# Performance work log

Hardware: AMD Instinct MI355X
Metric: run time of the kernel (lower is better)

Reference implementation:

```python
import jax, jax.numpy as jnp
import numpy as np

EMBED = 1024
HEADS = 16
HEAD_DIM = EMBED // HEADS


def setup_inputs() -> dict:
    key = jax.random.key(0)
    ks = jax.random.split(key, 12)
    B, S = 2, 2048
    inp = {
        "query": jax.random.normal(ks[0], (B, S, EMBED), dtype=jnp.float32),
        "key": jax.random.normal(ks[1], (B, S, EMBED), dtype=jnp.float32),
        "value": jax.random.normal(ks[2], (B, S, EMBED), dtype=jnp.float32),
        "mask": jnp.ones((B, 1, 1, S), dtype=jnp.int32),
    }
    scale = 1.0 / np.sqrt(EMBED)
    inp["Wq"] = jax.random.normal(ks[3], (EMBED, EMBED), dtype=jnp.float32) * scale
    inp["bq"] = jax.random.normal(ks[4], (EMBED,), dtype=jnp.float32) * 0.01
    inp["Wk"] = jax.random.normal(ks[5], (EMBED, EMBED), dtype=jnp.float32) * scale
    inp["bk"] = jax.random.normal(ks[6], (EMBED,), dtype=jnp.float32) * 0.01
    inp["Wv"] = jax.random.normal(ks[7], (EMBED, EMBED), dtype=jnp.float32) * scale
    inp["bv"] = jax.random.normal(ks[8], (EMBED,), dtype=jnp.float32) * 0.01
    inp["Wo"] = jax.random.normal(ks[9], (EMBED, EMBED), dtype=jnp.float32) * scale
    inp["bo"] = jax.random.normal(ks[10], (EMBED,), dtype=jnp.float32) * 0.01
    return inp


def reference(query, key, value, mask, Wq, bq, Wk, bk, Wv, bv, Wo, bo):
    N, Lq, _ = query.shape
    Lk = key.shape[1]
    # Linear projections (torch Linear: x @ W.T + b)
    q = (query @ Wq.T + bq).reshape(N, Lq, HEADS, HEAD_DIM)
    k = (key @ Wk.T + bk).reshape(N, Lk, HEADS, HEAD_DIM)
    v = (value @ Wv.T + bv).reshape(N, Lk, HEADS, HEAD_DIM)
    # scores: [N, H, Lq, Lk]
    energy = jnp.einsum("nqhd,nkhd->nhqk", q, k)
    energy = jnp.where(mask == 0, jnp.float32(-1e20), energy)
    # NOTE: original scales by sqrt(embedSize), not sqrt(head_dim)
    attn = jax.nn.softmax(energy / jnp.sqrt(jnp.float32(EMBED)), axis=3)
    out = jnp.einsum("nhqv,nvhd->nqhd", attn, v).reshape(N, Lq, EMBED)
    return out @ Wo.T + bo
```

## Files before the change

kernel.cpp:

```cpp
#include <hip/hip_runtime.h>
#include <stdint.h>

typedef unsigned short u16;
typedef __attribute__((ext_vector_type(8))) short short8;
typedef __attribute__((ext_vector_type(4))) short short4v;
typedef __attribute__((ext_vector_type(4))) float floatx4;
typedef __attribute__((ext_vector_type(16))) float floatx16;
typedef __attribute__((ext_vector_type(2))) unsigned int uint2v;
typedef __attribute__((ext_vector_type(4))) unsigned int uint4v;

#define AS_GLOBAL __attribute__((address_space(1)))
#define AS_LDS    __attribute__((address_space(3)))

#define QSCALE 0.045084220f

__device__ __forceinline__ float bf2f(u16 u) {
  union { unsigned int i; float f; } x; x.i = ((unsigned int)u) << 16; return x.f;
}
__device__ __forceinline__ u16 f2bf(float f) {
  union { float f; unsigned int i; } x; x.f = f;
  unsigned int u = x.i;
  u += 0x7fffu + ((u >> 16) & 1u);
  return (u16)(u >> 16);
}
__device__ __forceinline__ u16 f2bf_fast(float f) {
  union { float f; unsigned int i; } x; x.f = f;
  return (u16)((x.i + 0x8000u) >> 16);
}

__device__ __forceinline__ unsigned int cvtpk_bf16(float lo, float hi) {
  unsigned int w;
  __asm__("v_cvt_pk_bf16_f32 %0, %1, %2" : "=v"(w) : "v"(lo), "v"(hi));
  return w;
}

__device__ __forceinline__ void pl32_swap(unsigned int& a, unsigned int& b) {
#if __has_builtin(__builtin_amdgcn_permlane32_swap)
  uint2v r = __builtin_amdgcn_permlane32_swap(a, b, false, false);
  a = r[0]; b = r[1];
#else
  __asm__("v_permlane32_swap_b32 %0, %1" : "+v"(a), "+v"(b));
#endif
}

__device__ __forceinline__ int probe_is_f32(const void* p) {
  const unsigned int* w = (const unsigned int*)p;
  int cnt = 0;
#pragma unroll
  for (int i = 0; i < 64; ++i) {
    unsigned int lo = w[i] & 0xFFFFu;
    int e = (int)((lo >> 7) & 0xFFu);
    cnt += (e >= 117 && e <= 137) ? 1 : 0;
  }
  return cnt < 32;
}

__device__ __forceinline__ short8 ld8(const void* P, size_t off, int isf32) {
  if (isf32) {
    const float* q = (const float*)P + off;
    float4 x = *(const float4*)q;
    float4 y = *(const float4*)(q + 4);
    short8 r;
    r[0] = (short)f2bf(x.x); r[1] = (short)f2bf(x.y);
    r[2] = (short)f2bf(x.z); r[3] = (short)f2bf(x.w);
    r[4] = (short)f2bf(y.x); r[5] = (short)f2bf(y.y);
    r[6] = (short)f2bf(y.z); r[7] = (short)f2bf(y.w);
    return r;
  }
  return *(const short8*)((const u16*)P + off);
}

__device__ __forceinline__ float ldscalar(const void* P, size_t idx, int isf32) {
  return isf32 ? ((const float*)P)[idx] : bf2f(((const u16*)P)[idx]);
}

__global__ __launch_bounds__(256) void cvt7(
    const void* s0, const void* s1, const void* s2, const void* s3,
    const void* s4, const void* s5, const void* s6,
    u16* d0, u16* d1, u16* d2, u16* d3, u16* d4, u16* d5, u16* d6)
{
  const int z = blockIdx.y;
  const void* src; u16* dst; int n;
  switch (z) {
    case 0: src = s0; dst = d0; n = 4194304; break;
    case 1: src = s1; dst = d1; n = 4194304; break;
    case 2: src = s2; dst = d2; n = 4194304; break;
    case 3: src = s3; dst = d3; n = 1048576; break;
    case 4: src = s4; dst = d4; n = 1048576; break;
    case 5: src = s5; dst = d5; n = 1048576; break;
    default: src = s6; dst = d6; n = 1048576; break;
  }
  const int isf32 = probe_is_f32(src);
  for (int i = blockIdx.x * 256 + threadIdx.x; i * 4 < n; i += gridDim.x * 256) {
    if (isf32) {
      float4 x = ((const float4*)src)[i];
      short4v r;
      r[0] = (short)f2bf(x.x); r[1] = (short)f2bf(x.y);
      r[2] = (short)f2bf(x.z); r[3] = (short)f2bf(x.w);
      *(short4v*)(dst + (size_t)i * 4) = r;
    } else {
      *(short4v*)(dst + (size_t)i * 4) = ((const short4v*)src)[i];
    }
  }
}

__device__ __forceinline__ void gemm_core_bf16(
    const u16* __restrict__ A, const u16* __restrict__ W,
    u16* As, u16* Bs, floatx4 acc[4][4], int m0, int n0, int K, int tid)
{
  const int lane = tid & 63, wv = tid >> 6;
  const int wm = wv >> 1, wn = wv & 1;
  const int g = lane >> 4, ml = lane & 15;
  const int r0 = tid >> 2, kc = (tid & 3) << 3;
  const u16* Ag0 = A + (size_t)(m0 + r0) * K + kc;
  const u16* Ag1 = A + (size_t)(m0 + r0 + 64) * K + kc;
  const u16* Bg0 = W + (size_t)(n0 + r0) * K + kc;
  const u16* Bg1 = W + (size_t)(n0 + r0 + 64) * K + kc;

#define STAGE_QKV(buf_, kt_) do {                                              \
    u16* a0 = As + (buf_) * 4096 + tid * 8;                                    \
    u16* b0 = Bs + (buf_) * 4096 + tid * 8;                                    \
    __builtin_amdgcn_global_load_lds((const AS_GLOBAL unsigned int*)(Ag0 + (kt_)), \
                                     (AS_LDS unsigned int*)a0, 16, 0, 0);      \
    __builtin_amdgcn_global_load_lds((const AS_GLOBAL unsigned int*)(Ag1 + (kt_)), \
                                     (AS_LDS unsigned int*)(a0 + 2048), 16, 0, 0); \
    __builtin_amdgcn_global_load_lds((const AS_GLOBAL unsigned int*)(Bg0 + (kt_)), \
                                     (AS_LDS unsigned int*)b0, 16, 0, 0);      \
    __builtin_amdgcn_global_load_lds((const AS_GLOBAL unsigned int*)(Bg1 + (kt_)), \
                                     (AS_LDS unsigned int*)(b0 + 2048), 16, 0, 0); \
  } while (0)

  STAGE_QKV(0, 0);
  int buf = 0;
#pragma unroll 2
  for (int kt = 0; kt < K; kt += 32) {
    const int nk = (kt + 32 < K) ? (kt + 32) : 0;
    STAGE_QKV(buf ^ 1, nk);
    __asm__ __volatile__("s_waitcnt vmcnt(4)\n\ts_barrier" ::: "memory");
    const u16* Ac = As + buf * 4096;
    const u16* Bc = Bs + buf * 4096;
    short8 af[4], bf[4];
#pragma unroll
    for (int i = 0; i < 4; ++i)
      af[i] = *(const short8*)(Ac + (wm * 64 + i * 16 + ml) * 32 + g * 8);
#pragma unroll
    for (int j = 0; j < 4; ++j)
      bf[j] = *(const short8*)(Bc + (wn * 64 + j * 16 + ml) * 32 + g * 8);
#pragma unroll
    for (int i = 0; i < 4; ++i)
#pragma unroll
      for (int j = 0; j < 4; ++j)
        acc[i][j] = __builtin_amdgcn_mfma_f32_16x16x32_bf16(af[i], bf[j], acc[i][j], 0, 0, 0);
    __asm__ __volatile__("s_waitcnt lgkmcnt(0)\n\ts_barrier" ::: "memory");
    buf ^= 1;
  }
#undef STAGE_QKV
  __asm__ __volatile__("s_waitcnt vmcnt(0)" ::: "memory");
}

__device__ __forceinline__ void gemm_core_cvt(
    const void* __restrict__ A, const void* __restrict__ W, int aF32, int bF32,
    u16* As, u16* Bs, floatx4 acc[4][4], int m0, int n0, int K, int tid)
{
  const int lane = tid & 63, wv = tid >> 6;
  const int wm = wv >> 1, wn = wv & 1;
  const int g = lane >> 4, ml = lane & 15;
  const int r0 = tid >> 2, kc = (tid & 3) << 3;
  const size_t offA0 = (size_t)(m0 + r0) * K + kc;
  const size_t offA1 = (size_t)(m0 + r0 + 64) * K + kc;
  const size_t offB0 = (size_t)(n0 + r0) * K + kc;
  const size_t offB1 = (size_t)(n0 + r0 + 64) * K + kc;
  u16* Al0 = As + tid * 8;  u16* Al1 = As + (tid + 256) * 8;
  u16* Bl0 = Bs + tid * 8;  u16* Bl1 = Bs + (tid + 256) * 8;
  for (int kt = 0; kt < K; kt += 32) {
    short8 a0 = ld8(A, offA0 + kt, aF32);
    short8 a1 = ld8(A, offA1 + kt, aF32);
    short8 b0 = ld8(W, offB0 + kt, bF32);
    short8 b1 = ld8(W, offB1 + kt, bF32);
    *(short8*)Al0 = a0;  *(short8*)Al1 = a1;
    *(short8*)Bl0 = b0;  *(short8*)Bl1 = b1;
    __syncthreads();
    short8 af[4], bf[4];
#pragma unroll
    for (int i = 0; i < 4; ++i)
      af[i] = *(const short8*)(As + (wm * 64 + i * 16 + ml) * 32 + g * 8);
#pragma unroll
    for (int j = 0; j < 4; ++j)
      bf[j] = *(const short8*)(Bs + (wn * 64 + j * 16 + ml) * 32 + g * 8);
#pragma unroll
    for (int i = 0; i < 4; ++i)
#pragma unroll
      for (int j = 0; j < 4; ++j)
        acc[i][j] = __builtin_amdgcn_mfma_f32_16x16x32_bf16(af[i], bf[j], acc[i][j], 0, 0, 0);
    __syncthreads();
  }
}

__device__ __forceinline__ void qkv_epilogue(
    floatx4 acc[4][4], const void* Bi, int cF32, u16* O, int m0, int n0,
    int tid, int z)
{
  const int lane = tid & 63, wv = tid >> 6;
  const int wm = wv >> 1, wn = wv & 1, g = lane >> 4, ml = lane & 15;
  const float sc = (z == 0) ? QSCALE : 1.0f;
#pragma unroll
  for (int j = 0; j < 4; ++j) {
    int gn = n0 + wn * 64 + j * 16 + ml;
    float bvv = ldscalar(Bi, (size_t)gn, cF32);
    int h = gn >> 6, d = gn & 63;
    if (z == 2) {
#pragma unroll
      for (int i = 0; i < 4; ++i) {
        int gm0 = m0 + wm * 64 + i * 16 + g * 4;
        int b = gm0 >> 11, s0 = gm0 & 2047;
        short4v pk;
#pragma unroll
        for (int r = 0; r < 4; ++r) pk[r] = (short)f2bf_fast(acc[i][j][r] + bvv);
        *(short4v*)(O + ((((size_t)b * 16 + h) * 64 + d) * 2048 + s0)) = pk;
      }
    } else {
#pragma unroll
      for (int i = 0; i < 4; ++i)
#pragma unroll
        for (int r = 0; r < 4; ++r) {
          int gm = m0 + wm * 64 + i * 16 + g * 4 + r;
          int b = gm >> 11, s = gm & 2047;
          O[(((size_t)b * 16 + h) * 2048 + s) * 64 + d] =
              f2bf_fast((acc[i][j][r] + bvv) * sc);
        }
    }
  }
}

__global__ __launch_bounds__(256) void qkv_gemm_bf16(
    const u16* __restrict__ Xq, const u16* __restrict__ Xk, const u16* __restrict__ Xv,
    const u16* __restrict__ Wq, const u16* __restrict__ Wk, const u16* __restrict__ Wv,
    const void* __restrict__ Bq, const void* __restrict__ Bk, const void* __restrict__ Bv,
    u16* __restrict__ Oq, u16* __restrict__ Ok, u16* __restrict__ Ov)
{
  __align__(16) __shared__ u16 As[8192];
  __align__(16) __shared__ u16 Bs[8192];
  const int z = blockIdx.z;
  const u16* X = (z == 0) ? Xq : (z == 1) ? Xk : Xv;
  const u16* W = (z == 0) ? Wq : (z == 1) ? Wk : Wv;
  const void* Bi = (z == 0) ? Bq : (z == 1) ? Bk : Bv;
  u16* O = (z == 0) ? Oq : (z == 1) ? Ok : Ov;
  const int tid = threadIdx.x;
  const int m0 = blockIdx.x * 128, n0 = blockIdx.y * 128;
  floatx4 acc[4][4] = {};
  gemm_core_bf16(X, W, As, Bs, acc, m0, n0, 1024, tid);
  const int cF32 = probe_is_f32(Bi);
  qkv_epilogue(acc, Bi, cF32, O, m0, n0, tid, z);
}

__global__ __launch_bounds__(256) void qkv_gemm_cvt(
    const void* __restrict__ Xq, const void* __restrict__ Xk, const void* __restrict__ Xv,
    const void* __restrict__ Wq, const void* __restrict__ Wk, const void* __restrict__ Wv,
    const void* __restrict__ Bq, const void* __restrict__ Bk, const void* __restrict__ Bv,
    u16* __restrict__ Oq, u16* __restrict__ Ok, u16* __restrict__ Ov)
{
  __align__(16) __shared__ u16 As[4096];
  __align__(16) __shared__ u16 Bs[4096];
  const int z = blockIdx.z;
  const void* X  = (z == 0) ? Xq : (z == 1) ? Xk : Xv;
  const void* W  = (z == 0) ? Wq : (z == 1) ? Wk : Wv;
  const void* Bi = (z == 0) ? Bq : (z == 1) ? Bk : Bv;
  u16* O = (z == 0) ? Oq : (z == 1) ? Ok : Ov;
  const int aF32 = probe_is_f32(X);
  const int bF32 = probe_is_f32(W);
  const int cF32 = probe_is_f32(Bi);
  const int tid = threadIdx.x;
  const int m0 = blockIdx.y * 128, n0 = blockIdx.x * 128;
  floatx4 acc[4][4] = {};
  gemm_core_cvt(X, W, aF32, bF32, As, Bs, acc, m0, n0, 1024, tid);
  qkv_epilogue(acc, Bi, cF32, O, m0, n0, tid, z);
}

__global__ __launch_bounds__(256) void out_gemm_bf16(
    const u16* __restrict__ X, const u16* __restrict__ W,
    const void* __restrict__ Bi, float* __restrict__ O)
{
  __align__(16) __shared__ u16 As[8192];
  __align__(16) __shared__ u16 Bs[8192];
  const int tid = threadIdx.x;
  const int m0 = blockIdx.x * 128, n0 = blockIdx.y * 128;
  floatx4 acc[4][4] = {};
  gemm_core_bf16(X, W, As, Bs, acc, m0, n0, 1024, tid);
  const int cF32 = probe_is_f32(Bi);
  const int lane = tid & 63, wv = tid >> 6;
  const int wm = wv >> 1, wn = wv & 1, g = lane >> 4, ml = lane & 15;
#pragma unroll
  for (int j = 0; j < 4; ++j) {
    int gn = n0 + wn * 64 + j * 16 + ml;
    float bvv = ldscalar(Bi, (size_t)gn, cF32);
#pragma unroll
    for (int i = 0; i < 4; ++i)
#pragma unroll
      for (int r = 0; r < 4; ++r) {
        int gm = m0 + wm * 64 + i * 16 + g * 4 + r;
        O[(size_t)gm * 1024 + gn] = acc[i][j][r] + bvv;
      }
  }
}

__global__ __launch_bounds__(256) void out_gemm_cvt(
    const u16* __restrict__ X, const void* __restrict__ W,
    const void* __restrict__ Bi, float* __restrict__ O)
{
  __align__(16) __shared__ u16 As[4096];
  __align__(16) __shared__ u16 Bs[4096];
  const int bF32 = probe_is_f32(W);
  const int cF32 = probe_is_f32(Bi);
  const int tid = threadIdx.x;
  const int m0 = blockIdx.y * 128, n0 = blockIdx.x * 128;
  floatx4 acc[4][4] = {};
  gemm_core_cvt(X, W, 0, bF32, As, Bs, acc, m0, n0, 1024, tid);
  const int lane = tid & 63, wv = tid >> 6;
  const int wm = wv >> 1, wn = wv & 1, g = lane >> 4, ml = lane & 15;
#pragma unroll
  for (int j = 0; j < 4; ++j) {
    int gn = n0 + wn * 64 + j * 16 + ml;
    float bvv = ldscalar(Bi, (size_t)gn, cF32);
#pragma unroll
    for (int i = 0; i < 4; ++i)
#pragma unroll
      for (int r = 0; r < 4; ++r) {
        int gm = m0 + wm * 64 + i * 16 + g * 4 + r;
        O[(size_t)gm * 1024 + gn] = acc[i][j][r] + bvv;
      }
  }
}

__global__ __launch_bounds__(128) void flash_attn(
    const u16* __restrict__ Q, const u16* __restrict__ K, const u16* __restrict__ V,
    const int* __restrict__ Mask, u16* __restrict__ O)
{
  __align__(16) __shared__ u16 Ks[2][64 * 64];
  __align__(16) __shared__ u16 Vt[64 * 64];
  __align__(16) __shared__ int Ms[64];
  __shared__ int Wok[2];

  const int qt = blockIdx.x;
  const int bh = blockIdx.y;
  const int b = bh >> 4, h = bh & 15;
  const int tid = threadIdx.x;
  const int lane = tid & 63, wv = tid >> 6;
  const int H = lane >> 5, lq = lane & 31;
  const int koff = lq * 16 + H * 8;

  const size_t baseQ  = (((size_t)b * 16 + h) * 2048 + (size_t)qt * 64) * 64;
  const size_t baseKV = ((size_t)b * 16 + h) * 2048 * 64;

  {
    int la = 1;
#pragma unroll
    for (int i = 0; i < 16; ++i) la &= Mask[b * 2048 + tid * 16 + i];
    int wall = __all(la != 0);
    if (lane == 0) Wok[wv] = wall;
  }

  short8 qf[4];
  {
    const u16* qb = Q + baseQ + (size_t)(wv * 32 + lq) * 64 + H * 8;
#pragma unroll
    for (int c = 0; c < 4; ++c)
      qf[c] = *(const short8*)(qb + c * 16);
  }

  const u16* kg[4]; const u16* vg[4];
  int lo[4];
#pragma unroll
  for (int t = 0; t < 4; ++t) {
    int s = tid + t * 128;
    int blk = s >> 8;
    int ch  = (s >> 6) & 3;
    int row = (s >> 1) & 31;
    int hh  = s & 1;
    kg[t] = K + baseKV + (size_t)(blk * 32 + row) * 64 + ch * 16 + hh * 8;
    vg[t] = V + baseKV + (size_t)(blk * 32 + row) * 2048 + ch * 16 + hh * 8;
    lo[t] = ((tid & 64) + t * 128) * 8;
  }

#pragma unroll
  for (int t = 0; t < 4; ++t)
    __builtin_amdgcn_global_load_lds((const AS_GLOBAL unsigned int*)kg[t],
                                     (AS_LDS unsigned int*)(&Ks[0][0] + lo[t]), 16, 0, 0);

  __syncthreads();
  const bool maskall = Wok[0] && Wok[1];

  floatx16 oacc0 = {}, oacc1 = {};
  float lp = 0.f;

  int buf = 0;
#pragma unroll 2
  for (int kv0 = 0; kv0 < 2048; kv0 += 64) {
#pragma unroll
    for (int t = 0; t < 4; ++t)
      __builtin_amdgcn_global_load_lds((const AS_GLOBAL unsigned int*)(vg[t] + kv0),
                                       (AS_LDS unsigned int*)(Vt + lo[t]), 16, 0, 0);
    const int nxt = (kv0 + 64) & 2047;
#pragma unroll
    for (int t = 0; t < 4; ++t)
      __builtin_amdgcn_global_load_lds((const AS_GLOBAL unsigned int*)(kg[t] + (size_t)nxt * 64),
                                       (AS_LDS unsigned int*)(&Ks[buf ^ 1][0] + lo[t]), 16, 0, 0);
    if (!maskall && tid < 64) Ms[tid] = Mask[b * 2048 + kv0 + tid];
    __asm__ __volatile__("s_waitcnt vmcnt(8) lgkmcnt(0)\n\ts_barrier" ::: "memory");

    const u16* Kc = &Ks[buf][0];
    floatx16 a0 = {}, a1 = {};
    __builtin_amdgcn_s_setprio(1);
#pragma unroll
    for (int c = 0; c < 4; ++c) {
      short8 kb = *(const short8*)(Kc + c * 512 + koff);
      a0 = __builtin_amdgcn_mfma_f32_32x32x16_bf16(kb, qf[c], a0, 0, 0, 0);
    }
#pragma unroll
    for (int c = 0; c < 4; ++c) {
      short8 kb = *(const short8*)(Kc + (4 + c) * 512 + koff);
      a1 = __builtin_amdgcn_mfma_f32_32x32x16_bf16(kb, qf[c], a1, 0, 0, 0);
    }
    __builtin_amdgcn_s_setprio(0);

    float sv0[16], sv1[16];
#pragma unroll
    for (int r = 0; r < 16; ++r) { sv0[r] = a0[r]; sv1[r] = a1[r]; }
    if (!maskall) {
#pragma unroll
      for (int r = 0; r < 16; ++r) {
        int ko = (r & 3) + 8 * (r >> 2) + 4 * H;
        if (Ms[ko] == 0)      sv0[r] = -1.0e30f;
        if (Ms[32 + ko] == 0) sv1[r] = -1.0e30f;
      }
    }
#pragma unroll
    for (int r = 0; r < 16; ++r) {
      float p0 = __builtin_amdgcn_exp2f(sv0[r]);
      float p1 = __builtin_amdgcn_exp2f(sv1[r]);
      sv0[r] = p0; sv1[r] = p1;
      lp += p0 + p1;
    }

    unsigned int Wd0[8], Wd1[8];
#pragma unroll
    for (int i = 0; i < 8; ++i) {
      Wd0[i] = cvtpk_bf16(sv0[2 * i], sv0[2 * i + 1]);
      Wd1[i] = cvtpk_bf16(sv1[2 * i], sv1[2 * i + 1]);
    }
    short8 pa[4];
#define MAKE_PA(dst_, Wsrc_, base_) do {                                       \
    unsigned int u0 = Wsrc_[base_],     u1 = Wsrc_[(base_) + 1];               \
    unsigned int v0 = Wsrc_[(base_) + 2], v1 = Wsrc_[(base_) + 3];             \
    pl32_swap(u0, v0); pl32_swap(u1, v1);                                      \
    uint4v pw; pw[0] = u0; pw[1] = u1; pw[2] = v0; pw[3] = v1;                 \
    dst_ = __builtin_bit_cast(short8, pw);                                     \
  } while (0)
    MAKE_PA(pa[0], Wd0, 0);
    MAKE_PA(pa[1], Wd0, 4);
    MAKE_PA(pa[2], Wd1, 0);
    MAKE_PA(pa[3], Wd1, 4);
#undef MAKE_PA

    __asm__ __volatile__("s_waitcnt vmcnt(4)\n\ts_barrier" ::: "memory");

    __builtin_amdgcn_s_setprio(1);
#pragma unroll
    for (int c = 0; c < 4; ++c) {
      short8 vb = *(const short8*)(Vt + c * 512 + koff);
      oacc0 = __builtin_amdgcn_mfma_f32_32x32x16_bf16(pa[c], vb, oacc0, 0, 0, 0);
    }
#pragma unroll
    for (int c = 0; c < 4; ++c) {
      short8 vb = *(const short8*)(Vt + (4 + c) * 512 + koff);
      oacc1 = __builtin_amdgcn_mfma_f32_32x32x16_bf16(pa[c], vb, oacc1, 0, 0, 0);
    }
    __builtin_amdgcn_s_setprio(0);

    __asm__ __volatile__("s_barrier" ::: "memory");
    buf ^= 1;
  }
  __asm__ __volatile__("s_waitcnt vmcnt(0)" ::: "memory");

  float l = lp + __shfl_xor(lp, 32);
  float inv = (l > 0.f) ? 1.0f / l : 0.f;

#pragma unroll
  for (int r = 0; r < 16; ++r) {
    int qo = (r & 3) + 8 * (r >> 2) + 4 * H;
    float ivr = __shfl(inv, qo);
    int q = qt * 64 + wv * 32 + qo;
    size_t orow = ((size_t)b * 2048 + q) * 1024 + (size_t)h * 64;
    O[orow + lq]      = f2bf_fast(oacc0[r] * ivr);
    O[orow + 32 + lq] = f2bf_fast(oacc1[r] * ivr);
  }
}

extern "C" void kernel_launch(void* const* d_in, const int* in_sizes, int n_in,
                              void* d_out, int out_size, void* d_ws, size_t ws_size,
                              hipStream_t stream) {
  const void* q_in = d_in[0];
  const void* k_in = d_in[1];
  const void* v_in = d_in[2];
  const int* mask = (const int*)d_in[3];
  const void* Wq = d_in[4];  const void* bq = d_in[5];
  const void* Wk = d_in[6];  const void* bk = d_in[7];
  const void* Wv = d_in[8];  const void* bv = d_in[9];
  const void* Wo = d_in[10]; const void* bo = d_in[11];

  const size_t NTOK = (size_t)2 * 2048 * 1024;
  const size_t NW   = (size_t)1024 * 1024;

  if (ws_size >= (size_t)67108864) {
    u16* CXq = (u16*)d_ws;
    u16* CXk = CXq + NTOK;
    u16* CXv = CXk + NTOK;
    u16* CWq = CXv + NTOK;
    u16* CWk = CWq + NW;
    u16* CWv = CWk + NW;
    u16* CWo = CWv + NW;
    u16* Qp  = CWo + NW;
    u16* Kp  = Qp + NTOK;
    u16* Vp  = Kp + NTOK;
    u16* Ao  = Vp + NTOK;

    cvt7<<<dim3(1024, 7), 256, 0, stream>>>(q_in, k_in, v_in, Wq, Wk, Wv, Wo,
                                            CXq, CXk, CXv, CWq, CWk, CWv, CWo);
    qkv_gemm_bf16<<<dim3(32, 8, 3), 256, 0, stream>>>(CXq, CXk, CXv,
                                                      CWq, CWk, CWv,
                                                      bq, bk, bv, Qp, Kp, Vp);
    flash_attn<<<dim3(32, 32), 128, 0, stream>>>(Qp, Kp, Vp, mask, Ao);
    out_gemm_bf16<<<dim3(32, 8), 256, 0, stream>>>(Ao, CWo, bo, (float*)d_out);
  } else {
    u16* Qp = (u16*)d_ws;
    u16* Kp = Qp + NTOK;
    u16* Vp = Kp + NTOK;
    u16* Ao  = Vp + NTOK;

    qkv_gemm_cvt<<<dim3(8, 32, 3), 256, 0, stream>>>(q_in, k_in, v_in,
                                                     Wq, Wk, Wv, bq, bk, bv,
                                                     Qp, Kp, Vp);
    flash_attn<<<dim3(32, 32), 128, 0, stream>>>(Qp, Kp, Vp, mask, Ao);
    out_gemm_cvt<<<dim3(8, 32), 256, 0, stream>>>(Ao, Wo, bo, (float*)d_out);
  }
}
```

Measured before the change: 252.5 us.

## Split flash attention KV tiles across four waves with LDS cross-wave reduction

The flash attention block grows from 2 to 4 waves. Each pair of waves takes half of every 64-key tile (split-K within the tile), so the per-wave MFMA, exp and pack work is halved. The partial output accumulators and row sums are combined through LDS at the end, which reuses the K buffer. This raises the number of waves available to hide latency, at the cost of an extra reduction step with two barriers and more threads contending on the same per-tile barriers.

After: 246.4 us. -2.4%, faster.

```diff
diff --git a/kernel.cpp b/kernel.cpp
--- a/kernel.cpp
+++ b/kernel.cpp
@@ -331,20 +331,22 @@
   }
 }
 
-__global__ __launch_bounds__(128) void flash_attn(
+__global__ __launch_bounds__(256, 4) void flash_attn(
     const u16* __restrict__ Q, const u16* __restrict__ K, const u16* __restrict__ V,
     const int* __restrict__ Mask, u16* __restrict__ O)
 {
   __align__(16) __shared__ u16 Ks[2][64 * 64];
   __align__(16) __shared__ u16 Vt[64 * 64];
   __align__(16) __shared__ int Ms[64];
-  __shared__ int Wok[2];
+  __align__(16) __shared__ float Lf[256];
+  __shared__ int Wok[4];
 
   const int qt = blockIdx.x;
   const int bh = blockIdx.y;
   const int b = bh >> 4, h = bh & 15;
   const int tid = threadIdx.x;
   const int lane = tid & 63, wv = tid >> 6;
+  const int qh = wv & 1, kh = wv >> 1;
   const int H = lane >> 5, lq = lane & 31;
   const int koff = lq * 16 + H * 8;
 
@@ -354,40 +356,40 @@
   {
     int la = 1;
 #pragma unroll
-    for (int i = 0; i < 16; ++i) la &= Mask[b * 2048 + tid * 16 + i];
+    for (int i = 0; i < 8; ++i) la &= Mask[b * 2048 + tid * 8 + i];
     int wall = __all(la != 0);
     if (lane == 0) Wok[wv] = wall;
   }
 
   short8 qf[4];
   {
-    const u16* qb = Q + baseQ + (size_t)(wv * 32 + lq) * 64 + H * 8;
+    const u16* qb = Q + baseQ + (size_t)(qh * 32 + lq) * 64 + H * 8;
 #pragma unroll
     for (int c = 0; c < 4; ++c)
       qf[c] = *(const short8*)(qb + c * 16);
   }
 
-  const u16* kg[4]; const u16* vg[4];
-  int lo[4];
-#pragma unroll
-  for (int t = 0; t < 4; ++t) {
-    int s = tid + t * 128;
+  const u16* kg[2]; const u16* vg[2];
+  int lo[2];
+#pragma unroll
+  for (int t = 0; t < 2; ++t) {
+    int s = tid + t * 256;
     int blk = s >> 8;
     int ch  = (s >> 6) & 3;
     int row = (s >> 1) & 31;
     int hh  = s & 1;
     kg[t] = K + baseKV + (size_t)(blk * 32 + row) * 64 + ch * 16 + hh * 8;
     vg[t] = V + baseKV + (size_t)(blk * 32 + row) * 2048 + ch * 16 + hh * 8;
-    lo[t] = ((tid & 64) + t * 128) * 8;
-  }
-
-#pragma unroll
-  for (int t = 0; t < 4; ++t)
+    lo[t] = ((tid & 192) + t * 256) * 8;
+  }
+
+#pragma unroll
+  for (int t = 0; t < 2; ++t)
     __builtin_amdgcn_global_load_lds((const AS_GLOBAL unsigned int*)kg[t],
                                      (AS_LDS unsigned int*)(&Ks[0][0] + lo[t]), 16, 0, 0);
 
   __syncthreads();
-  const bool maskall = Wok[0] && Wok[1];
+  const bool maskall = Wok[0] && Wok[1] && Wok[2] && Wok[3];
 
   floatx16 oacc0 = {}, oacc1 = {};
   float lp = 0.f;
@@ -396,82 +398,71 @@
 #pragma unroll 2
   for (int kv0 = 0; kv0 < 2048; kv0 += 64) {
 #pragma unroll
-    for (int t = 0; t < 4; ++t)
+    for (int t = 0; t < 2; ++t)
       __builtin_amdgcn_global_load_lds((const AS_GLOBAL unsigned int*)(vg[t] + kv0),
                                        (AS_LDS unsigned int*)(Vt + lo[t]), 16, 0, 0);
     const int nxt = (kv0 + 64) & 2047;
 #pragma unroll
-    for (int t = 0; t < 4; ++t)
+    for (int t = 0; t < 2; ++t)
       __builtin_amdgcn_global_load_lds((const AS_GLOBAL unsigned int*)(kg[t] + (size_t)nxt * 64),
                                        (AS_LDS unsigned int*)(&Ks[buf ^ 1][0] + lo[t]), 16, 0, 0);
     if (!maskall && tid < 64) Ms[tid] = Mask[b * 2048 + kv0 + tid];
-    __asm__ __volatile__("s_waitcnt vmcnt(8) lgkmcnt(0)\n\ts_barrier" ::: "memory");
+    __asm__ __volatile__("s_waitcnt vmcnt(4) lgkmcnt(0)\n\ts_barrier" ::: "memory");
 
     const u16* Kc = &Ks[buf][0];
-    floatx16 a0 = {}, a1 = {};
+    floatx16 a = {};
     __builtin_amdgcn_s_setprio(1);
 #pragma unroll
     for (int c = 0; c < 4; ++c) {
-      short8 kb = *(const short8*)(Kc + c * 512 + koff);
-      a0 = __builtin_amdgcn_mfma_f32_32x32x16_bf16(kb, qf[c], a0, 0, 0, 0);
-    }
-#pragma unroll
-    for (int c = 0; c < 4; ++c) {
-      short8 kb = *(const short8*)(Kc + (4 + c) * 512 + koff);
-      a1 = __builtin_amdgcn_mfma_f32_32x32x16_bf16(kb, qf[c], a1, 0, 0, 0);
+      short8 kb = *(const short8*)(Kc + (kh * 4 + c) * 512 + koff);
+      a = __builtin_amdgcn_mfma_f32_32x32x16_bf16(kb, qf[c], a, 0, 0, 0);
     }
     __builtin_amdgcn_s_setprio(0);
 
-    float sv0[16], sv1[16];
-#pragma unroll
-    for (int r = 0; r < 16; ++r) { sv0[r] = a0[r]; sv1[r] = a1[r]; }
+    float sv[16];
+#pragma unroll
+    for (int r = 0; r < 16; ++r) sv[r] = a[r];
     if (!maskall) {
 #pragma unroll
       for (int r = 0; r < 16; ++r) {
-        int ko = (r & 3) + 8 * (r >> 2) + 4 * H;
-        if (Ms[ko] == 0)      sv0[r] = -1.0e30f;
-        if (Ms[32 + ko] == 0) sv1[r] = -1.0e30f;
+        int ko = 32 * kh + (r & 3) + 8 * (r >> 2) + 4 * H;
+        if (Ms[ko] == 0) sv[r] = -1.0e30f;
       }
     }
 #pragma unroll
     for (int r = 0; r < 16; ++r) {
-      float p0 = __builtin_amdgcn_exp2f(sv0[r]);
-      float p1 = __builtin_amdgcn_exp2f(sv1[r]);
-      sv0[r] = p0; sv1[r] = p1;
-      lp += p0 + p1;
-    }
-
-    unsigned int Wd0[8], Wd1[8];
-#pragma unroll
-    for (int i = 0; i < 8; ++i) {
-      Wd0[i] = cvtpk_bf16(sv0[2 * i], sv0[2 * i + 1]);
-      Wd1[i] = cvtpk_bf16(sv1[2 * i], sv1[2 * i + 1]);
-    }
-    short8 pa[4];
+      float p = __builtin_amdgcn_exp2f(sv[r]);
+      sv[r] = p;
+      lp += p;
+    }
+
+    unsigned int Wd[8];
+#pragma unroll
+    for (int i = 0; i < 8; ++i)
+      Wd[i] = cvtpk_bf16(sv[2 * i], sv[2 * i + 1]);
+    short8 pa[2];
 #define MAKE_PA(dst_, Wsrc_, base_) do {                                       \
-    unsigned int u0 = Wsrc_[base_],     u1 = Wsrc_[(base_) + 1];               \
+    unsigned int u0 = Wsrc_[base_],       u1 = Wsrc_[(base_) + 1];             \
     unsigned int v0 = Wsrc_[(base_) + 2], v1 = Wsrc_[(base_) + 3];             \
     pl32_swap(u0, v0); pl32_swap(u1, v1);                                      \
     uint4v pw; pw[0] = u0; pw[1] = u1; pw[2] = v0; pw[3] = v1;                 \
     dst_ = __builtin_bit_cast(short8, pw);                                     \
   } while (0)
-    MAKE_PA(pa[0], Wd0, 0);
-    MAKE_PA(pa[1], Wd0, 4);
-    MAKE_PA(pa[2], Wd1, 0);
-    MAKE_PA(pa[3], Wd1, 4);
+    MAKE_PA(pa[0], Wd, 0);
+    MAKE_PA(pa[1], Wd, 4);
 #undef MAKE_PA
 
-    __asm__ __volatile__("s_waitcnt vmcnt(4)\n\ts_barrier" ::: "memory");
+    __asm__ __volatile__("s_waitcnt vmcnt(2)\n\ts_barrier" ::: "memory");
 
     __builtin_amdgcn_s_setprio(1);
 #pragma unroll
-    for (int c = 0; c < 4; ++c) {
-      short8 vb = *(const short8*)(Vt + c * 512 + koff);
+    for (int c = 0; c < 2; ++c) {
+      short8 vb = *(const short8*)(Vt + (2 * kh + c) * 512 + koff);
       oacc0 = __builtin_amdgcn_mfma_f32_32x32x16_bf16(pa[c], vb, oacc0, 0, 0, 0);
     }
 #pragma unroll
-    for (int c = 0; c < 4; ++c) {
-      short8 vb = *(const short8*)(Vt + (4 + c) * 512 + koff);
+    for (int c = 0; c < 2; ++c) {
+      short8 vb = *(const short8*)(Vt + (4 + 2 * kh + c) * 512 + koff);
       oacc1 = __builtin_amdgcn_mfma_f32_32x32x16_bf16(pa[c], vb, oacc1, 0, 0, 0);
     }
     __builtin_amdgcn_s_setprio(0);
@@ -480,18 +471,44 @@
     buf ^= 1;
   }
   __asm__ __volatile__("s_waitcnt vmcnt(0)" ::: "memory");
-
-  float l = lp + __shfl_xor(lp, 32);
+  __syncthreads();
+
+  float lh = lp + __shfl_xor(lp, 32);
+  Lf[wv * 64 + lane] = lh;
+  float* Xf = (float*)&Ks[0][0];
+  {
+    float* myreg = Xf + wv * 1024;
+    const floatx16& dep = kh ? oacc0 : oacc1;
+#pragma unroll
+    for (int w = 0; w < 4; ++w) {
+      float4 f4;
+      f4.x = dep[4 * w + 0]; f4.y = dep[4 * w + 1];
+      f4.z = dep[4 * w + 2]; f4.w = dep[4 * w + 3];
+      *(float4*)(myreg + w * 256 + lane * 4) = f4;
+    }
+  }
+  __syncthreads();
+  const int pwv = wv ^ 2;
+  float l = lh + Lf[pwv * 64 + lane];
   float inv = (l > 0.f) ? 1.0f / l : 0.f;
+  floatx16 mine = kh ? oacc1 : oacc0;
+  {
+    const float* prr = Xf + pwv * 1024;
+#pragma unroll
+    for (int w = 0; w < 4; ++w) {
+      float4 f4 = *(const float4*)(prr + w * 256 + lane * 4);
+      mine[4 * w + 0] += f4.x; mine[4 * w + 1] += f4.y;
+      mine[4 * w + 2] += f4.z; mine[4 * w + 3] += f4.w;
+    }
+  }
 
 #pragma unroll
   for (int r = 0; r < 16; ++r) {
     int qo = (r & 3) + 8 * (r >> 2) + 4 * H;
     float ivr = __shfl(inv, qo);
-    int q = qt * 64 + wv * 32 + qo;
+    int q = qt * 64 + qh * 32 + qo;
     size_t orow = ((size_t)b * 2048 + q) * 1024 + (size_t)h * 64;
-    O[orow + lq]      = f2bf_fast(oacc0[r] * ivr);
-    O[orow + 32 + lq] = f2bf_fast(oacc1[r] * ivr);
+    O[orow + kh * 32 + lq] = f2bf_fast(mine[r] * ivr);
   }
 }
 
@@ -528,7 +545,7 @@
     qkv_gemm_bf16<<<dim3(32, 8, 3), 256, 0, stream>>>(CXq, CXk, CXv,
                                                       CWq, CWk, CWv,
                                                       bq, bk, bv, Qp, Kp, Vp);
-    flash_attn<<<dim3(32, 32), 128, 0, stream>>>(Qp, Kp, Vp, mask, Ao);
+    flash_attn<<<dim3(32, 32), 256, 0, stream>>>(Qp, Kp, Vp, mask, Ao);
     out_gemm_bf16<<<dim3(32, 8), 256, 0, stream>>>(Ao, CWo, bo, (float*)d_out);
   } else {
     u16* Qp = (u16*)d_ws;
@@ -539,7 +556,7 @@
     qkv_gemm_cvt<<<dim3(8, 32, 3), 256, 0, stream>>>(q_in, k_in, v_in,
                                                      Wq, Wk, Wv, bq, bk, bv,
                                                      Qp, Kp, Vp);
-    flash_attn<<<dim3(32, 32), 128, 0, stream>>>(Qp, Kp, Vp, mask, Ao);
+    flash_attn<<<dim3(32, 32), 256, 0, stream>>>(Qp, Kp, Vp, mask, Ao);
     out_gemm_cvt<<<dim3(8, 32), 256, 0, stream>>>(Ao, Wo, bo, (float*)d_out);
   }
 }
```
